# Optimization experiments

Hardware: AMD Instinct MI355X
Metric: run time of the kernel (lower is better)

Reference implementation:

```python
import jax, jax.numpy as jnp
import numpy as np

N_NODES = 50000
N_EDGES = 800000
R = 3          # relations
D_IN = 96
D_HID = 96
D_OUT = 64


def setup_inputs() -> dict:
    key = jax.random.key(0)
    ks = jax.random.split(key, 10)
    s_in = 1.0 / np.sqrt(D_IN)
    s_hid = 1.0 / np.sqrt(D_HID)
    return {
        "x": jax.random.normal(ks[0], (N_NODES, D_IN), jnp.float32),
        "src": jax.random.randint(ks[1], (R, N_EDGES), 0, N_NODES, jnp.int32),
        "dst": jax.random.randint(ks[2], (R, N_EDGES), 0, N_NODES, jnp.int32),
        "Ws1": jax.random.normal(ks[3], (R, D_IN, D_HID), jnp.float32) * s_in,
        "Wn1": jax.random.normal(ks[4], (R, D_IN, D_HID), jnp.float32) * s_in,
        "b1": jnp.zeros((R, D_HID), jnp.float32),
        "Ws2": jax.random.normal(ks[5], (R, D_HID, D_OUT), jnp.float32) * s_hid,
        "Wn2": jax.random.normal(ks[6], (R, D_HID, D_OUT), jnp.float32) * s_hid,
        "b2": jnp.zeros((R, D_OUT), jnp.float32),
    }


def reference(x, src, dst, Ws1, Wn1, b1, Ws2, Wn2, b2):
    N = x.shape[0]
    # in-degree per relation, clamped to 1 (DGL zero-in-degree convention)
    deg = jax.vmap(lambda d: jax.ops.segment_sum(
        jnp.ones(d.shape[0], x.dtype), d, num_segments=N))(dst)        # [R, N]
    inv_deg = (1.0 / jnp.maximum(deg, 1.0))[..., None]                 # [R, N, 1]

    def sage_layer(h, Ws, Wn, b):
        # gather src feats, mean-aggregate onto dst, per relation
        neigh = jax.vmap(lambda s, d: jax.ops.segment_sum(
            h[s], d, num_segments=N))(src, dst) * inv_deg              # [R, N, Din]
        out = jnp.tanh(
            jnp.einsum('nd,rdh->rnh', h, Ws)
            + jnp.einsum('rnd,rdh->rnh', neigh, Wn)
            + b[:, None, :])                                           # [R, N, H]
        return out.mean(axis=0)  # HeteroGraphConv aggregate='mean'

    h1 = sage_layer(x, Ws1, Wn1, b1)
    return sage_layer(h1, Ws2, Wn2, b2)
```

## Files before the change

kernel.cpp:

```cpp
#include <hip/hip_runtime.h>
#include <hip/hip_bf16.h>

constexpr int NN   = 50000;
constexpr int NE   = 800000;
constexpr int NR   = 3;
constexpr int DIN  = 96;
constexpr int DH   = 96;
constexpr int DOUT = 64;
constexpr int SLOT = 64;
constexpr int ZROW = NN;

constexpr int NBUCK   = 196;
constexpr int LCAP    = 56;
constexpr int P1B     = 256;
constexpr int CHUNK   = NE / P1B;
constexpr int BSTRIDE = 3200;
constexpr int LSTRIDE = 200;

constexpr int SCAT_BLKS = NR * P1B;
constexpr int CONV_BLKS = (NN * 96 + 4095) / 4096;
constexpr int WT_ELEMS  = 2 * NR * DIN * DH + 2 * NR * DH * DOUT;
constexpr int WT_BLKS   = (WT_ELEMS + 511) / 512;
constexpr int PREP_GRID = SCAT_BLKS + CONV_BLKS + WT_BLKS;

typedef __attribute__((ext_vector_type(8))) short bf16x8;
typedef __attribute__((ext_vector_type(4))) float f32x4;

__device__ __forceinline__ unsigned short f2b(float f) {
    unsigned int u = __float_as_uint(f);
    u += 0x7fffu + ((u >> 16) & 1u);
    return (unsigned short)(u >> 16);
}
__device__ __forceinline__ float blo(unsigned int u) { return __uint_as_float(u << 16); }
__device__ __forceinline__ float bhi(unsigned int u) { return __uint_as_float(u & 0xffff0000u); }
__device__ __forceinline__ unsigned int pack2(float lo, float hi) {
    return (unsigned int)f2b(lo) | ((unsigned int)f2b(hi) << 16);
}

struct __align__(4) U3 { unsigned int x, y, z; };

__global__ __launch_bounds__(512)
void prep_kernel(const int* __restrict__ src,
                 const int* __restrict__ dst,
                 unsigned int* __restrict__ gbuck,
                 int* __restrict__ glofs,
                 const float* __restrict__ x,
                 unsigned short* __restrict__ xb,
                 const float* __restrict__ Ws1, const float* __restrict__ Wn1,
                 const float* __restrict__ Ws2, const float* __restrict__ Wn2,
                 unsigned short* __restrict__ wt)
{
    __shared__ unsigned int lbuf[NBUCK][LCAP];
    __shared__ int lcnt[NBUCK];
    __shared__ int sa[256], sb[256];
    __shared__ int lofs[NBUCK + 1];

    const int bid = blockIdx.x;
    const int tid = threadIdx.x;

    if (bid < SCAT_BLKS) {
        const int r = bid >> 8, c = bid & 255;
        for (int i = tid; i < NBUCK; i += 512) lcnt[i] = 0;
        __syncthreads();

        const int* sr = src + (size_t)r * NE + (size_t)c * CHUNK;
        const int* dr = dst + (size_t)r * NE + (size_t)c * CHUNK;
        for (int i = tid; i < CHUNK; i += 512) {
            int d = dr[i];
            int s = sr[i];
            int b = d >> 8;
            int pos = atomicAdd(&lcnt[b], 1);
            if (pos < LCAP)
                lbuf[b][pos] = ((unsigned int)(d & 255) << 16) | (unsigned int)s;
        }
        __syncthreads();

        if (tid < 256)
            sa[tid] = (tid < NBUCK) ? min(lcnt[tid], LCAP) : 0;
        __syncthreads();
        int* cur = sa; int* nxt = sb;
        for (int st = 1; st < 256; st <<= 1) {
            if (tid < 256) {
                int v = cur[tid];
                if (tid >= st) v += cur[tid - st];
                nxt[tid] = v;
            }
            __syncthreads();
            int* t2 = cur; cur = nxt; nxt = t2;
        }
        if (tid == 0) lofs[0] = 0;
        if (tid < NBUCK) lofs[tid + 1] = cur[tid];
        __syncthreads();

        if (tid < NBUCK + 1) glofs[(size_t)bid * LSTRIDE + tid] = lofs[tid];

        const int w = tid >> 6, l = tid & 63;
        unsigned int* gb = gbuck + (size_t)bid * BSTRIDE;
        for (int b = w; b < NBUCK; b += 8) {
            int cnt = min(lcnt[b], LCAP);
            if (l < cnt) gb[lofs[b] + l] = lbuf[b][l];
        }
    } else if (bid < SCAT_BLKS + CONV_BLKS) {
        const int rb = bid - SCAT_BLKS;
        if (rb == 0 && tid < 48) {
            unsigned int* z = reinterpret_cast<unsigned int*>(xb + (size_t)ZROW * 96);
            z[tid] = 0u;
        }
        int i = (rb * 512 + tid) * 8;
        if (i < NN * 96) {
            float4 a = *reinterpret_cast<const float4*>(x + i);
            float4 b = *reinterpret_cast<const float4*>(x + i + 4);
            uint4 o;
            o.x = pack2(a.x, a.y);
            o.y = pack2(a.z, a.w);
            o.z = pack2(b.x, b.y);
            o.w = pack2(b.z, b.w);
            *reinterpret_cast<uint4*>(xb + i) = o;
        }
    } else {
        int g = (bid - SCAT_BLKS - CONV_BLKS) * 512 + tid;
        if (g < WT_ELEMS) {
            constexpr int SZ1 = NR * DIN * DH;
            constexpr int SZ2 = NR * DH * DOUT;
            const float* in;
            int idx, KD, ND;
            if (g < SZ1)                { in = Ws1; idx = g;                KD = DIN; ND = DH; }
            else if (g < 2 * SZ1)       { in = Wn1; idx = g - SZ1;          KD = DIN; ND = DH; }
            else if (g < 2 * SZ1 + SZ2) { in = Ws2; idx = g - 2 * SZ1;      KD = DH;  ND = DOUT; }
            else                        { in = Wn2; idx = g - 2 * SZ1 - SZ2; KD = DH; ND = DOUT; }
            int k = idx % KD;
            int rn = idx / KD;
            int n = rn % ND;
            int r = rn / ND;
            wt[g] = f2b(in[((size_t)r * KD + k) * ND + n]);
        }
    }
}

__global__ __launch_bounds__(512)
void bin_build_kernel(const unsigned int* __restrict__ gbuck,
                      const int* __restrict__ glofs,
                      unsigned short* __restrict__ slots,
                      int* __restrict__ deg)
{
    __shared__ unsigned short lslot[256][SLOT];
    __shared__ int lcnt[256];

    const int rb = blockIdx.x;
    const int r  = rb / NBUCK, b = rb - r * NBUCK;
    const int nbase = b * 256;
    int nb = NN - nbase; if (nb > 256) nb = 256;
    const int tid = threadIdx.x;

    unsigned int* ls32i = reinterpret_cast<unsigned int*>(&lslot[0][0]);
    for (int i = tid; i < 256 * SLOT / 2; i += 512) ls32i[i] = 0xC350C350u;
    for (int i = tid; i < 256; i += 512) lcnt[i] = 0;
    __syncthreads();

    const int blk  = tid >> 1;
    const int half = tid & 1;
    const int gblk = r * P1B + blk;
    int o0 = glofs[(size_t)gblk * LSTRIDE + b];
    int o1 = glofs[(size_t)gblk * LSTRIDE + b + 1];
    const unsigned int* run = gbuck + (size_t)gblk * BSTRIDE + o0;
    int cnt = o1 - o0;
    for (int i = half; i < cnt; i += 2) {
        unsigned int e = run[i];
        int nl = e >> 16;
        int pos = atomicAdd(&lcnt[nl], 1);
        if (pos < SLOT) lslot[nl][pos] = (unsigned short)(e & 0xffffu);
    }
    __syncthreads();

    for (int j = tid; j < nb; j += 512) deg[r * NN + nbase + j] = lcnt[j];

    const unsigned int* ls32 = reinterpret_cast<const unsigned int*>(&lslot[0][0]);
    unsigned int* gs32 = reinterpret_cast<unsigned int*>(
        slots + ((size_t)r * NN + nbase) * SLOT);
    const int tot = nb * (SLOT / 2);
    for (int i = tid; i < tot; i += 512) gs32[i] = ls32[i];
}

__global__ __launch_bounds__(256)
void agg_kernel(const unsigned int* __restrict__ Hb,
                const unsigned short* __restrict__ slots,
                const int* __restrict__ deg,
                unsigned int* __restrict__ aggb)
{
    int gid = blockIdx.x * 256 + threadIdx.x;
    int grp = gid >> 4, t = gid & 15;
    if (grp >= NR * NN) return;
    const uint4* sl4 = reinterpret_cast<const uint4*>(slots + (size_t)grp * SLOT);
    int e = deg[grp];
    if (e > SLOT) e = SLOT;

    uint4 iv0 = sl4[0], iv1 = sl4[1], iv2 = sl4[2], iv3 = sl4[3];

    float a0 = 0.f, a1 = 0.f, a2 = 0.f, a3 = 0.f, a4 = 0.f, a5 = 0.f;

#define DO8(V)                                                                 \
    {                                                                          \
        unsigned int i0 = (V).x & 0xffffu, i1 = (V).x >> 16;                   \
        unsigned int i2 = (V).y & 0xffffu, i3 = (V).y >> 16;                   \
        unsigned int i4 = (V).z & 0xffffu, i5 = (V).z >> 16;                   \
        unsigned int i6 = (V).w & 0xffffu, i7 = (V).w >> 16;                   \
        U3 g0 = *reinterpret_cast<const U3*>(Hb + (size_t)i0 * 48 + 3 * t);    \
        U3 g1 = *reinterpret_cast<const U3*>(Hb + (size_t)i1 * 48 + 3 * t);    \
        U3 g2 = *reinterpret_cast<const U3*>(Hb + (size_t)i2 * 48 + 3 * t);    \
        U3 g3 = *reinterpret_cast<const U3*>(Hb + (size_t)i3 * 48 + 3 * t);    \
        U3 g4 = *reinterpret_cast<const U3*>(Hb + (size_t)i4 * 48 + 3 * t);    \
        U3 g5 = *reinterpret_cast<const U3*>(Hb + (size_t)i5 * 48 + 3 * t);    \
        U3 g6 = *reinterpret_cast<const U3*>(Hb + (size_t)i6 * 48 + 3 * t);    \
        U3 g7 = *reinterpret_cast<const U3*>(Hb + (size_t)i7 * 48 + 3 * t);    \
        a0 += blo(g0.x) + blo(g1.x) + blo(g2.x) + blo(g3.x)                    \
            + blo(g4.x) + blo(g5.x) + blo(g6.x) + blo(g7.x);                   \
        a1 += bhi(g0.x) + bhi(g1.x) + bhi(g2.x) + bhi(g3.x)                    \
            + bhi(g4.x) + bhi(g5.x) + bhi(g6.x) + bhi(g7.x);                   \
        a2 += blo(g0.y) + blo(g1.y) + blo(g2.y) + blo(g3.y)                    \
            + blo(g4.y) + blo(g5.y) + blo(g6.y) + blo(g7.y);                   \
        a3 += bhi(g0.y) + bhi(g1.y) + bhi(g2.y) + bhi(g3.y)                    \
            + bhi(g4.y) + bhi(g5.y) + bhi(g6.y) + bhi(g7.y);                   \
        a4 += blo(g0.z) + blo(g1.z) + blo(g2.z) + blo(g3.z)                    \
            + blo(g4.z) + blo(g5.z) + blo(g6.z) + blo(g7.z);                   \
        a5 += bhi(g0.z) + bhi(g1.z) + bhi(g2.z) + bhi(g3.z)                    \
            + bhi(g4.z) + bhi(g5.z) + bhi(g6.z) + bhi(g7.z);                   \
    }

    int nb8 = (e + 7) >> 3;
    if (nb8 > 0) DO8(iv0);
    if (nb8 > 1) DO8(iv1);
    if (nb8 > 2) DO8(iv2);
    if (nb8 > 3) DO8(iv3);
    for (int i = 32; i < e; i += 8) {
        uint4 v = sl4[i >> 3];
        DO8(v);
    }
#undef DO8

    float inv = 1.0f / (float)(e > 0 ? e : 1);
    unsigned int* o = aggb + (size_t)grp * 48 + 3 * t;
    o[0] = pack2(a0 * inv, a1 * inv);
    o[1] = pack2(a2 * inv, a3 * inv);
    o[2] = pack2(a4 * inv, a5 * inv);
}

template <int NOUT, bool OUT16>
__global__ __launch_bounds__(256)
void mfma_layer_kernel(const unsigned short* Hb,
                       const unsigned short* __restrict__ aggb,
                       const unsigned short* __restrict__ Wts,
                       const unsigned short* __restrict__ Wtn,
                       const float* __restrict__ bias,
                       unsigned short* o16,
                       float* __restrict__ o32)
{
    const int w    = threadIdx.x >> 6;
    const int l    = threadIdx.x & 63;
    const int n0   = blockIdx.x * 64 + w * 16;
    const int arow = l & 15, asel = l >> 4;
    int na = n0 + arow;
    if (na > NN - 1) na = NN - 1;

    bf16x8 ax[3], ag[NR][3];
    {
        const unsigned short* xr = Hb + (size_t)na * 96 + asel * 8;
        #pragma unroll
        for (int kb = 0; kb < 3; ++kb)
            ax[kb] = *reinterpret_cast<const bf16x8*>(xr + kb * 32);
        #pragma unroll
        for (int r = 0; r < NR; ++r) {
            const unsigned short* gr = aggb + ((size_t)r * NN + na) * 96 + asel * 8;
            #pragma unroll
            for (int kb = 0; kb < 3; ++kb)
                ag[r][kb] = *reinterpret_cast<const bf16x8*>(gr + kb * 32);
        }
    }

    constexpr int NC = NOUT / 16;
    #pragma unroll
    for (int c = 0; c < NC; ++c) {
        f32x4 acc[NR];
        #pragma unroll
        for (int r = 0; r < NR; ++r) acc[r] = (f32x4){0.f, 0.f, 0.f, 0.f};

        #pragma unroll
        for (int r = 0; r < NR; ++r) {
            const unsigned short* bs = Wts + ((size_t)r * NOUT + c * 16 + arow) * 96 + asel * 8;
            const unsigned short* bn = Wtn + ((size_t)r * NOUT + c * 16 + arow) * 96 + asel * 8;
            #pragma unroll
            for (int kb = 0; kb < 3; ++kb) {
                acc[r] = __builtin_amdgcn_mfma_f32_16x16x32_bf16(
                    ax[kb], *reinterpret_cast<const bf16x8*>(bs + kb * 32), acc[r], 0, 0, 0);
                acc[r] = __builtin_amdgcn_mfma_f32_16x16x32_bf16(
                    ag[r][kb], *reinterpret_cast<const bf16x8*>(bn + kb * 32), acc[r], 0, 0, 0);
            }
        }

        const int col = c * 16 + arow;
        const float b0 = bias[col];
        const float b1 = bias[NOUT + col];
        const float b2 = bias[2 * NOUT + col];
        #pragma unroll
        for (int j = 0; j < 4; ++j) {
            int node = n0 + asel * 4 + j;
            if (node < NN) {
                float v = (tanhf(acc[0][j] + b0) + tanhf(acc[1][j] + b1)
                         + tanhf(acc[2][j] + b2)) * (1.0f / 3.0f);
                if (OUT16) o16[(size_t)node * 96 + col] = f2b(v);
                else       o32[(size_t)node * DOUT + col] = v;
            }
        }
    }
}

extern "C" void kernel_launch(void* const* d_in, const int* in_sizes, int n_in,
                              void* d_out, int out_size, void* d_ws, size_t ws_size,
                              hipStream_t stream)
{
    const float* x   = (const float*)d_in[0];
    const int*   src = (const int*)d_in[1];
    const int*   dst = (const int*)d_in[2];
    const float* Ws1 = (const float*)d_in[3];
    const float* Wn1 = (const float*)d_in[4];
    const float* b1  = (const float*)d_in[5];
    const float* Ws2 = (const float*)d_in[6];
    const float* Wn2 = (const float*)d_in[7];
    const float* b2  = (const float*)d_in[8];
    float* out = (float*)d_out;

    char* ws = (char*)d_ws;
    size_t o = 0;
    auto alloc = [&](size_t bytes) {
        size_t p = o;
        o += (bytes + 255) & ~(size_t)255;
        return p;
    };
    int* deg = (int*)(ws + alloc((size_t)NR * NN * 4));
    unsigned short* slots = (unsigned short*)(ws + alloc((size_t)NR * NN * SLOT * 2));
    unsigned short* xb = (unsigned short*)(ws + alloc((size_t)(NN + 1) * 96 * 2));
    unsigned short* aggb = (unsigned short*)(ws + alloc((size_t)NR * NN * 96 * 2));
    unsigned short* wt = (unsigned short*)(ws + alloc((size_t)WT_ELEMS * 2));
    unsigned short* wt1s = wt;
    unsigned short* wt1n = wt1s + NR * DIN * DH;
    unsigned short* wt2s = wt1n + NR * DIN * DH;
    unsigned short* wt2n = wt2s + NR * DH * DOUT;
    unsigned int* gbuck = (unsigned int*)aggb;
    int* glofs = (int*)((char*)aggb + (size_t)NR * P1B * BSTRIDE * 4);

    prep_kernel<<<PREP_GRID, 512, 0, stream>>>(
        src, dst, gbuck, glofs, x, xb, Ws1, Wn1, Ws2, Wn2, wt);

    bin_build_kernel<<<NR * NBUCK, 512, 0, stream>>>(gbuck, glofs, slots, deg);

    constexpr int AGG_GRID  = NR * NN * 16 / 256;
    constexpr int GEMM_GRID = (NN + 63) / 64;

    agg_kernel<<<AGG_GRID, 256, 0, stream>>>(
        (const unsigned int*)xb, slots, deg, (unsigned int*)aggb);
    mfma_layer_kernel<DH, true><<<GEMM_GRID, 256, 0, stream>>>(
        xb, aggb, wt1s, wt1n, b1, xb, (float*)nullptr);

    agg_kernel<<<AGG_GRID, 256, 0, stream>>>(
        (const unsigned int*)xb, slots, deg, (unsigned int*)aggb);
    mfma_layer_kernel<DOUT, false><<<GEMM_GRID, 256, 0, stream>>>(
        xb, aggb, wt2s, wt2n, b2, (unsigned short*)nullptr, out);
}
```

Measured before the change: 210.8 us.

## Transform-before-aggregate in layer 2 and degree-sorted aggregation ordering

Layer 2 now projects h1 through Wn2 per relation first (y2_kernel, 96 to 64 features) and then gathers and averages the 64-wide rows, exploiting linearity of mean aggregation. This shrinks gather traffic and removes the neighbor MFMAs from the final layer kernel, at the cost of an extra GEMM pass and an intermediate buffer. It also adds per-bucket sorting of nodes by in-degree in bin_build, and the aggregation kernels walk nodes in that order so wavefronts see similar degrees and diverge less. The fast path runs only if the workspace is large enough, with a fallback to the old path otherwise.

```diff
diff --git a/kernel.cpp b/kernel.cpp
--- a/kernel.cpp
+++ b/kernel.cpp
@@ -16,6 +16,7 @@
 constexpr int CHUNK   = NE / P1B;
 constexpr int BSTRIDE = 3200;
 constexpr int LSTRIDE = 200;
+constexpr int NWIN    = NR * NBUCK;
 
 constexpr int SCAT_BLKS = NR * P1B;
 constexpr int CONV_BLKS = (NN * 96 + 4095) / 4096;
@@ -124,10 +125,10 @@
             constexpr int SZ2 = NR * DH * DOUT;
             const float* in;
             int idx, KD, ND;
-            if (g < SZ1)                { in = Ws1; idx = g;                KD = DIN; ND = DH; }
-            else if (g < 2 * SZ1)       { in = Wn1; idx = g - SZ1;          KD = DIN; ND = DH; }
-            else if (g < 2 * SZ1 + SZ2) { in = Ws2; idx = g - 2 * SZ1;      KD = DH;  ND = DOUT; }
-            else                        { in = Wn2; idx = g - 2 * SZ1 - SZ2; KD = DH; ND = DOUT; }
+            if (g < SZ1)                { in = Ws1; idx = g;                 KD = DIN; ND = DH; }
+            else if (g < 2 * SZ1)       { in = Wn1; idx = g - SZ1;           KD = DIN; ND = DH; }
+            else if (g < 2 * SZ1 + SZ2) { in = Ws2; idx = g - 2 * SZ1;       KD = DH;  ND = DOUT; }
+            else                        { in = Wn2; idx = g - 2 * SZ1 - SZ2; KD = DH;  ND = DOUT; }
             int k = idx % KD;
             int rn = idx / KD;
             int n = rn % ND;
@@ -141,10 +142,12 @@
 void bin_build_kernel(const unsigned int* __restrict__ gbuck,
                       const int* __restrict__ glofs,
                       unsigned short* __restrict__ slots,
-                      int* __restrict__ deg)
+                      int* __restrict__ deg,
+                      unsigned short* __restrict__ order)
 {
     __shared__ unsigned short lslot[256][SLOT];
     __shared__ int lcnt[256];
+    __shared__ unsigned short sord[256];
 
     const int rb = blockIdx.x;
     const int r  = rb / NBUCK, b = rb - r * NBUCK;
@@ -155,6 +158,7 @@
     unsigned int* ls32i = reinterpret_cast<unsigned int*>(&lslot[0][0]);
     for (int i = tid; i < 256 * SLOT / 2; i += 512) ls32i[i] = 0xC350C350u;
     for (int i = tid; i < 256; i += 512) lcnt[i] = 0;
+    if (tid < 128) reinterpret_cast<unsigned int*>(sord)[tid] = 0xFFFFFFFFu;
     __syncthreads();
 
     const int blk  = tid >> 1;
@@ -174,6 +178,23 @@
 
     for (int j = tid; j < nb; j += 512) deg[r * NN + nbase + j] = lcnt[j];
 
+    if (tid < 256) {
+        const int j = tid;
+        const int myk = (j < nb) ? lcnt[j] : -1;
+        int rank = 0;
+        #pragma unroll 8
+        for (int k = 0; k < 256; ++k) {
+            int kk = (k < nb) ? lcnt[k] : -1;
+            rank += (kk > myk) || (kk == myk && k < j);
+        }
+        if (j < nb) sord[rank] = (unsigned short)j;
+    }
+    __syncthreads();
+
+    if (tid < 128)
+        reinterpret_cast<unsigned int*>(order + (size_t)rb * 256)[tid] =
+            reinterpret_cast<const unsigned int*>(sord)[tid];
+
     const unsigned int* ls32 = reinterpret_cast<const unsigned int*>(&lslot[0][0]);
     unsigned int* gs32 = reinterpret_cast<unsigned int*>(
         slots + ((size_t)r * NN + nbase) * SLOT);
@@ -181,21 +202,35 @@
     for (int i = tid; i < tot; i += 512) gs32[i] = ls32[i];
 }
 
+__device__ __forceinline__ bool agg_decode(const unsigned short* __restrict__ order,
+                                           int g, int& r, int& node, int& grp)
+{
+    int rb = g >> 8;
+    int ordv = order[g];
+    if (ordv == 0xFFFF) return false;
+    r = rb / NBUCK;
+    int b = rb - r * NBUCK;
+    node = (b << 8) + ordv;
+    grp = r * NN + node;
+    return true;
+}
+
 __global__ __launch_bounds__(256)
-void agg_kernel(const unsigned int* __restrict__ Hb,
-                const unsigned short* __restrict__ slots,
-                const int* __restrict__ deg,
-                unsigned int* __restrict__ aggb)
+void agg96_kernel(const unsigned int* __restrict__ Hb,
+                  const unsigned short* __restrict__ slots,
+                  const int* __restrict__ deg,
+                  const unsigned short* __restrict__ order,
+                  unsigned int* __restrict__ aggb)
 {
     int gid = blockIdx.x * 256 + threadIdx.x;
-    int grp = gid >> 4, t = gid & 15;
-    if (grp >= NR * NN) return;
+    int g = gid >> 4, t = gid & 15;
+    int r, node, grp;
+    if (!agg_decode(order, g, r, node, grp)) return;
     const uint4* sl4 = reinterpret_cast<const uint4*>(slots + (size_t)grp * SLOT);
     int e = deg[grp];
     if (e > SLOT) e = SLOT;
 
     uint4 iv0 = sl4[0], iv1 = sl4[1], iv2 = sl4[2], iv3 = sl4[3];
-
     float a0 = 0.f, a1 = 0.f, a2 = 0.f, a3 = 0.f, a4 = 0.f, a5 = 0.f;
 
 #define DO8(V)                                                                 \
@@ -244,16 +279,76 @@
     o[2] = pack2(a4 * inv, a5 * inv);
 }
 
-template <int NOUT, bool OUT16>
 __global__ __launch_bounds__(256)
-void mfma_layer_kernel(const unsigned short* Hb,
-                       const unsigned short* __restrict__ aggb,
-                       const unsigned short* __restrict__ Wts,
-                       const unsigned short* __restrict__ Wtn,
-                       const float* __restrict__ bias,
-                       unsigned short* o16,
-                       float* __restrict__ o32)
-{
+void agg64_kernel(const unsigned int* __restrict__ y2,
+                  const unsigned short* __restrict__ slots,
+                  const int* __restrict__ deg,
+                  const unsigned short* __restrict__ order,
+                  unsigned int* __restrict__ aggY2)
+{
+    int gid = blockIdx.x * 256 + threadIdx.x;
+    int g = gid >> 4, t = gid & 15;
+    int r, node, grp;
+    if (!agg_decode(order, g, r, node, grp)) return;
+    const unsigned int* Tp = y2 + (size_t)r * ((size_t)(NN + 1) * 32);
+    const uint4* sl4 = reinterpret_cast<const uint4*>(slots + (size_t)grp * SLOT);
+    int e = deg[grp];
+    if (e > SLOT) e = SLOT;
+
+    uint4 iv0 = sl4[0], iv1 = sl4[1], iv2 = sl4[2], iv3 = sl4[3];
+    float a0 = 0.f, a1 = 0.f, a2 = 0.f, a3 = 0.f;
+
+#define DO8W(V)                                                                \
+    {                                                                          \
+        unsigned int i0 = (V).x & 0xffffu, i1 = (V).x >> 16;                   \
+        unsigned int i2 = (V).y & 0xffffu, i3 = (V).y >> 16;                   \
+        unsigned int i4 = (V).z & 0xffffu, i5 = (V).z >> 16;                   \
+        unsigned int i6 = (V).w & 0xffffu, i7 = (V).w >> 16;                   \
+        uint2 g0 = *reinterpret_cast<const uint2*>(Tp + (size_t)i0 * 32 + 2 * t); \
+        uint2 g1 = *reinterpret_cast<const uint2*>(Tp + (size_t)i1 * 32 + 2 * t); \
+        uint2 g2 = *reinterpret_cast<const uint2*>(Tp + (size_t)i2 * 32 + 2 * t); \
+        uint2 g3 = *reinterpret_cast<const uint2*>(Tp + (size_t)i3 * 32 + 2 * t); \
+        uint2 g4 = *reinterpret_cast<const uint2*>(Tp + (size_t)i4 * 32 + 2 * t); \
+        uint2 g5 = *reinterpret_cast<const uint2*>(Tp + (size_t)i5 * 32 + 2 * t); \
+        uint2 g6 = *reinterpret_cast<const uint2*>(Tp + (size_t)i6 * 32 + 2 * t); \
+        uint2 g7 = *reinterpret_cast<const uint2*>(Tp + (size_t)i7 * 32 + 2 * t); \
+        a0 += blo(g0.x) + blo(g1.x) + blo(g2.x) + blo(g3.x)                    \
+            + blo(g4.x) + blo(g5.x) + blo(g6.x) + blo(g7.x);                   \
+        a1 += bhi(g0.x) + bhi(g1.x) + bhi(g2.x) + bhi(g3.x)                    \
+            + bhi(g4.x) + bhi(g5.x) + bhi(g6.x) + bhi(g7.x);                   \
+        a2 += blo(g0.y) + blo(g1.y) + blo(g2.y) + blo(g3.y)                    \
+            + blo(g4.y) + blo(g5.y) + blo(g6.y) + blo(g7.y);                   \
+        a3 += bhi(g0.y) + bhi(g1.y) + bhi(g2.y) + bhi(g3.y)                    \
+            + bhi(g4.y) + bhi(g5.y) + bhi(g6.y) + bhi(g7.y);                   \
+    }
+
+    int nb8 = (e + 7) >> 3;
+    if (nb8 > 0) DO8W(iv0);
+    if (nb8 > 1) DO8W(iv1);
+    if (nb8 > 2) DO8W(iv2);
+    if (nb8 > 3) DO8W(iv3);
+    for (int i = 32; i < e; i += 8) {
+        uint4 v = sl4[i >> 3];
+        DO8W(v);
+    }
+#undef DO8W
+
+    float inv = 1.0f / (float)(e > 0 ? e : 1);
+    unsigned int* o = aggY2 + (size_t)grp * 32 + 2 * t;
+    o[0] = pack2(a0 * inv, a1 * inv);
+    o[1] = pack2(a2 * inv, a3 * inv);
+}
+
+__global__ __launch_bounds__(256)
+void y2_kernel(const unsigned short* __restrict__ Hb,
+               const unsigned short* __restrict__ Wtn,
+               unsigned short* __restrict__ y2)
+{
+    if (blockIdx.x == 0 && threadIdx.x < 96) {
+        unsigned int* z = reinterpret_cast<unsigned int*>(y2);
+        int r = threadIdx.x >> 5, d = threadIdx.x & 31;
+        z[((size_t)r * (NN + 1) + ZROW) * 32 + d] = 0u;
+    }
     const int w    = threadIdx.x >> 6;
     const int l    = threadIdx.x & 63;
     const int n0   = blockIdx.x * 64 + w * 16;
@@ -261,42 +356,107 @@
     int na = n0 + arow;
     if (na > NN - 1) na = NN - 1;
 
+    bf16x8 ax[3];
+    const unsigned short* xr = Hb + (size_t)na * 96 + asel * 8;
+    #pragma unroll
+    for (int kb = 0; kb < 3; ++kb)
+        ax[kb] = *reinterpret_cast<const bf16x8*>(xr + kb * 32);
+
+    #pragma unroll
+    for (int c = 0; c < 4; ++c) {
+        f32x4 acc[NR];
+        #pragma unroll
+        for (int r = 0; r < NR; ++r) acc[r] = (f32x4){0.f, 0.f, 0.f, 0.f};
+        #pragma unroll
+        for (int r = 0; r < NR; ++r) {
+            const unsigned short* bn = Wtn + ((size_t)r * DOUT + c * 16 + arow) * 96 + asel * 8;
+            #pragma unroll
+            for (int kb = 0; kb < 3; ++kb)
+                acc[r] = __builtin_amdgcn_mfma_f32_16x16x32_bf16(
+                    ax[kb], *reinterpret_cast<const bf16x8*>(bn + kb * 32), acc[r], 0, 0, 0);
+        }
+        const int col = c * 16 + arow;
+        #pragma unroll
+        for (int r = 0; r < NR; ++r)
+            #pragma unroll
+            for (int j = 0; j < 4; ++j) {
+                int node = n0 + asel * 4 + j;
+                if (node < NN)
+                    y2[((size_t)r * (NN + 1) + node) * 64 + col] = f2b(acc[r][j]);
+            }
+    }
+}
+
+template <int NOUT, bool OUT16, bool PRE_AGG>
+__global__ __launch_bounds__(256)
+void mfma_layer_kernel(const unsigned short* Hb,
+                       const unsigned short* __restrict__ aggb,
+                       const unsigned short* __restrict__ aggY2,
+                       const unsigned short* __restrict__ Wts,
+                       const unsigned short* __restrict__ Wtn,
+                       const float* __restrict__ bias,
+                       unsigned short* o16,
+                       float* __restrict__ o32)
+{
+    const int w    = threadIdx.x >> 6;
+    const int l    = threadIdx.x & 63;
+    const int n0   = blockIdx.x * 64 + w * 16;
+    const int arow = l & 15, asel = l >> 4;
+    int na = n0 + arow;
+    if (na > NN - 1) na = NN - 1;
+
     bf16x8 ax[3], ag[NR][3];
     {
         const unsigned short* xr = Hb + (size_t)na * 96 + asel * 8;
         #pragma unroll
         for (int kb = 0; kb < 3; ++kb)
             ax[kb] = *reinterpret_cast<const bf16x8*>(xr + kb * 32);
-        #pragma unroll
-        for (int r = 0; r < NR; ++r) {
-            const unsigned short* gr = aggb + ((size_t)r * NN + na) * 96 + asel * 8;
+        if (!PRE_AGG) {
             #pragma unroll
-            for (int kb = 0; kb < 3; ++kb)
-                ag[r][kb] = *reinterpret_cast<const bf16x8*>(gr + kb * 32);
+            for (int r = 0; r < NR; ++r) {
+                const unsigned short* gr = aggb + ((size_t)r * NN + na) * 96 + asel * 8;
+                #pragma unroll
+                for (int kb = 0; kb < 3; ++kb)
+                    ag[r][kb] = *reinterpret_cast<const bf16x8*>(gr + kb * 32);
+            }
         }
     }
 
     constexpr int NC = NOUT / 16;
     #pragma unroll
     for (int c = 0; c < NC; ++c) {
+        const int col = c * 16 + arow;
         f32x4 acc[NR];
-        #pragma unroll
-        for (int r = 0; r < NR; ++r) acc[r] = (f32x4){0.f, 0.f, 0.f, 0.f};
+        if (PRE_AGG) {
+            #pragma unroll
+            for (int r = 0; r < NR; ++r)
+                #pragma unroll
+                for (int j = 0; j < 4; ++j) {
+                    int nj = n0 + asel * 4 + j;
+                    if (nj > NN - 1) nj = NN - 1;
+                    unsigned short hv = aggY2[((size_t)r * NN + nj) * NOUT + col];
+                    acc[r][j] = __uint_as_float((unsigned int)hv << 16);
+                }
+        } else {
+            #pragma unroll
+            for (int r = 0; r < NR; ++r) acc[r] = (f32x4){0.f, 0.f, 0.f, 0.f};
+        }
 
         #pragma unroll
         for (int r = 0; r < NR; ++r) {
             const unsigned short* bs = Wts + ((size_t)r * NOUT + c * 16 + arow) * 96 + asel * 8;
-            const unsigned short* bn = Wtn + ((size_t)r * NOUT + c * 16 + arow) * 96 + asel * 8;
             #pragma unroll
             for (int kb = 0; kb < 3; ++kb) {
                 acc[r] = __builtin_amdgcn_mfma_f32_16x16x32_bf16(
                     ax[kb], *reinterpret_cast<const bf16x8*>(bs + kb * 32), acc[r], 0, 0, 0);
-                acc[r] = __builtin_amdgcn_mfma_f32_16x16x32_bf16(
-                    ag[r][kb], *reinterpret_cast<const bf16x8*>(bn + kb * 32), acc[r], 0, 0, 0);
+                if (!PRE_AGG) {
+                    const unsigned short* bn = Wtn + ((size_t)r * NOUT + c * 16 + arow) * 96 + asel * 8;
+                    acc[r] = __builtin_amdgcn_mfma_f32_16x16x32_bf16(
+                        ag[r][kb], *reinterpret_cast<const bf16x8*>(bn + kb * 32), acc[r], 0, 0, 0);
+                }
             }
         }
 
-        const int col = c * 16 + arow;
         const float b0 = bias[col];
         const float b1 = bias[NOUT + col];
         const float b2 = bias[2 * NOUT + col];
@@ -340,28 +500,43 @@
     unsigned short* xb = (unsigned short*)(ws + alloc((size_t)(NN + 1) * 96 * 2));
     unsigned short* aggb = (unsigned short*)(ws + alloc((size_t)NR * NN * 96 * 2));
     unsigned short* wt = (unsigned short*)(ws + alloc((size_t)WT_ELEMS * 2));
+    unsigned short* order = (unsigned short*)(ws + alloc((size_t)NWIN * 256 * 2));
+    size_t need_base = o;
+    unsigned short* aggY2 = (unsigned short*)(ws + alloc((size_t)NR * NN * DOUT * 2));
+    size_t need_fast = o;
+    const bool fast2 = (ws_size >= need_fast);
+    (void)need_base;
+
     unsigned short* wt1s = wt;
     unsigned short* wt1n = wt1s + NR * DIN * DH;
     unsigned short* wt2s = wt1n + NR * DIN * DH;
     unsigned short* wt2n = wt2s + NR * DH * DOUT;
     unsigned int* gbuck = (unsigned int*)aggb;
     int* glofs = (int*)((char*)aggb + (size_t)NR * P1B * BSTRIDE * 4);
+    unsigned short* y2 = aggb;
 
     prep_kernel<<<PREP_GRID, 512, 0, stream>>>(
         src, dst, gbuck, glofs, x, xb, Ws1, Wn1, Ws2, Wn2, wt);
-
-    bin_build_kernel<<<NR * NBUCK, 512, 0, stream>>>(gbuck, glofs, slots, deg);
-
-    constexpr int AGG_GRID  = NR * NN * 16 / 256;
+    bin_build_kernel<<<NWIN, 512, 0, stream>>>(gbuck, glofs, slots, deg, order);
+
+    constexpr int AGG_GRID  = NWIN * 16;
     constexpr int GEMM_GRID = (NN + 63) / 64;
 
-    agg_kernel<<<AGG_GRID, 256, 0, stream>>>(
-        (const unsigned int*)xb, slots, deg, (unsigned int*)aggb);
-    mfma_layer_kernel<DH, true><<<GEMM_GRID, 256, 0, stream>>>(
-        xb, aggb, wt1s, wt1n, b1, xb, (float*)nullptr);
-
-    agg_kernel<<<AGG_GRID, 256, 0, stream>>>(
-        (const unsigned int*)xb, slots, deg, (unsigned int*)aggb);
-    mfma_layer_kernel<DOUT, false><<<GEMM_GRID, 256, 0, stream>>>(
-        xb, aggb, wt2s, wt2n, b2, (unsigned short*)nullptr, out);
-}
+    agg96_kernel<<<AGG_GRID, 256, 0, stream>>>(
+        (const unsigned int*)xb, slots, deg, order, (unsigned int*)aggb);
+    mfma_layer_kernel<DH, true, false><<<GEMM_GRID, 256, 0, stream>>>(
+        xb, aggb, nullptr, wt1s, wt1n, b1, xb, (float*)nullptr);
+
+    if (fast2) {
+        y2_kernel<<<GEMM_GRID, 256, 0, stream>>>(xb, wt2n, y2);
+        agg64_kernel<<<AGG_GRID, 256, 0, stream>>>(
+            (const unsigned int*)y2, slots, deg, order, (unsigned int*)aggY2);
+        mfma_layer_kernel<DOUT, false, true><<<GEMM_GRID, 256, 0, stream>>>(
+            xb, nullptr, aggY2, wt2s, wt2n, b2, (unsigned short*)nullptr, out);
+    } else {
+        agg96_kernel<<<AGG_GRID, 256, 0, stream>>>(
+            (const unsigned int*)xb, slots, deg, order, (unsigned int*)aggb);
+        mfma_layer_kernel<DOUT, false, false><<<GEMM_GRID, 256, 0, stream>>>(
+            xb, aggb, nullptr, wt2s, wt2n, b2, (unsigned short*)nullptr, out);
+    }
+}
```

Result: slower. 225.7 us (+7.0%).

## Slice aggregation by feature column across XCD-mapped blocks for L2 locality

Applied to the files above, without the earlier changes.

Replaces the aggregation kernel with a column-sliced version. Each block handles one third of the 96-wide feature row (16 dwords) for 16 destination groups. The block index is mapped so that blocks landing on different XCDs (blockIdx mod 8) work on a fixed slice, so each XCD's L2 caches only part of the source feature table. Slot-index loads and output stores become nontemporal to avoid polluting cache. The cost is three times as many slot/degree reads and a smaller 4-byte gather per lane, which may lower memory-level parallelism per thread.

```diff
diff --git a/kernel.cpp b/kernel.cpp
--- a/kernel.cpp
+++ b/kernel.cpp
@@ -23,8 +23,13 @@
 constexpr int WT_BLKS   = (WT_ELEMS + 511) / 512;
 constexpr int PREP_GRID = SCAT_BLKS + CONV_BLKS + WT_BLKS;
 
+constexpr int NGRP_BLKS  = NR * NN / 16;
+constexpr int AGG_ROUNDS = (NGRP_BLKS + 1) / 2;
+constexpr int AGGS_GRID  = AGG_ROUNDS * 8;
+
 typedef __attribute__((ext_vector_type(8))) short bf16x8;
 typedef __attribute__((ext_vector_type(4))) float f32x4;
+typedef __attribute__((ext_vector_type(4))) unsigned int uint4v;
 
 __device__ __forceinline__ unsigned short f2b(float f) {
     unsigned int u = __float_as_uint(f);
@@ -36,8 +41,6 @@
 __device__ __forceinline__ unsigned int pack2(float lo, float hi) {
     return (unsigned int)f2b(lo) | ((unsigned int)f2b(hi) << 16);
 }
-
-struct __align__(4) U3 { unsigned int x, y, z; };
 
 __global__ __launch_bounds__(512)
 void prep_kernel(const int* __restrict__ src,
@@ -124,10 +127,10 @@
             constexpr int SZ2 = NR * DH * DOUT;
             const float* in;
             int idx, KD, ND;
-            if (g < SZ1)                { in = Ws1; idx = g;                KD = DIN; ND = DH; }
-            else if (g < 2 * SZ1)       { in = Wn1; idx = g - SZ1;          KD = DIN; ND = DH; }
-            else if (g < 2 * SZ1 + SZ2) { in = Ws2; idx = g - 2 * SZ1;      KD = DH;  ND = DOUT; }
-            else                        { in = Wn2; idx = g - 2 * SZ1 - SZ2; KD = DH; ND = DOUT; }
+            if (g < SZ1)                { in = Ws1; idx = g;                 KD = DIN; ND = DH; }
+            else if (g < 2 * SZ1)       { in = Wn1; idx = g - SZ1;           KD = DIN; ND = DH; }
+            else if (g < 2 * SZ1 + SZ2) { in = Ws2; idx = g - 2 * SZ1;       KD = DH;  ND = DOUT; }
+            else                        { in = Wn2; idx = g - 2 * SZ1 - SZ2; KD = DH;  ND = DOUT; }
             int k = idx % KD;
             int rn = idx / KD;
             int n = rn % ND;
@@ -182,66 +185,69 @@
 }
 
 __global__ __launch_bounds__(256)
-void agg_kernel(const unsigned int* __restrict__ Hb,
-                const unsigned short* __restrict__ slots,
-                const int* __restrict__ deg,
-                unsigned int* __restrict__ aggb)
-{
-    int gid = blockIdx.x * 256 + threadIdx.x;
-    int grp = gid >> 4, t = gid & 15;
-    if (grp >= NR * NN) return;
-    const uint4* sl4 = reinterpret_cast<const uint4*>(slots + (size_t)grp * SLOT);
+void agg_sliced_kernel(const unsigned int* __restrict__ Hb,
+                       const unsigned short* __restrict__ slots,
+                       const int* __restrict__ deg,
+                       unsigned int* __restrict__ aggb)
+{
+    const int x = blockIdx.x & 7;
+    const int q = blockIdx.x >> 3;
+    const int s = (x * 3) >> 3;
+    const int nx = (s == 2) ? 2 : 3;
+    const int k = x - ((s == 0) ? 0 : (s == 1) ? 3 : 6);
+    const int j = q * nx + k;
+    if (j >= NGRP_BLKS) return;
+
+    const int tid = threadIdx.x;
+    const int grp = j * 16 + (tid >> 4);
+    const int t   = tid & 15;
+    const unsigned int* T = Hb + s * 16 + t;
+
+    const uint4v* sl4 = reinterpret_cast<const uint4v*>(slots + (size_t)grp * SLOT);
     int e = deg[grp];
     if (e > SLOT) e = SLOT;
 
-    uint4 iv0 = sl4[0], iv1 = sl4[1], iv2 = sl4[2], iv3 = sl4[3];
-
-    float a0 = 0.f, a1 = 0.f, a2 = 0.f, a3 = 0.f, a4 = 0.f, a5 = 0.f;
-
-#define DO8(V)                                                                 \
+    uint4v iv0 = __builtin_nontemporal_load(sl4 + 0);
+    uint4v iv1 = __builtin_nontemporal_load(sl4 + 1);
+    uint4v iv2 = __builtin_nontemporal_load(sl4 + 2);
+    uint4v iv3 = __builtin_nontemporal_load(sl4 + 3);
+
+    float a0 = 0.f, a1 = 0.f;
+
+#define DO8S(V)                                                                \
     {                                                                          \
         unsigned int i0 = (V).x & 0xffffu, i1 = (V).x >> 16;                   \
         unsigned int i2 = (V).y & 0xffffu, i3 = (V).y >> 16;                   \
         unsigned int i4 = (V).z & 0xffffu, i5 = (V).z >> 16;                   \
         unsigned int i6 = (V).w & 0xffffu, i7 = (V).w >> 16;                   \
-        U3 g0 = *reinterpret_cast<const U3*>(Hb + (size_t)i0 * 48 + 3 * t);    \
-        U3 g1 = *reinterpret_cast<const U3*>(Hb + (size_t)i1 * 48 + 3 * t);    \
-        U3 g2 = *reinterpret_cast<const U3*>(Hb + (size_t)i2 * 48 + 3 * t);    \
-        U3 g3 = *reinterpret_cast<const U3*>(Hb + (size_t)i3 * 48 + 3 * t);    \
-        U3 g4 = *reinterpret_cast<const U3*>(Hb + (size_t)i4 * 48 + 3 * t);    \
-        U3 g5 = *reinterpret_cast<const U3*>(Hb + (size_t)i5 * 48 + 3 * t);    \
-        U3 g6 = *reinterpret_cast<const U3*>(Hb + (size_t)i6 * 48 + 3 * t);    \
-        U3 g7 = *reinterpret_cast<const U3*>(Hb + (size_t)i7 * 48 + 3 * t);    \
-        a0 += blo(g0.x) + blo(g1.x) + blo(g2.x) + blo(g3.x)                    \
-            + blo(g4.x) + blo(g5.x) + blo(g6.x) + blo(g7.x);                   \
-        a1 += bhi(g0.x) + bhi(g1.x) + bhi(g2.x) + bhi(g3.x)                    \
-            + bhi(g4.x) + bhi(g5.x) + bhi(g6.x) + bhi(g7.x);                   \
-        a2 += blo(g0.y) + blo(g1.y) + blo(g2.y) + blo(g3.y)                    \
-            + blo(g4.y) + blo(g5.y) + blo(g6.y) + blo(g7.y);                   \
-        a3 += bhi(g0.y) + bhi(g1.y) + bhi(g2.y) + bhi(g3.y)                    \
-            + bhi(g4.y) + bhi(g5.y) + bhi(g6.y) + bhi(g7.y);                   \
-        a4 += blo(g0.z) + blo(g1.z) + blo(g2.z) + blo(g3.z)                    \
-            + blo(g4.z) + blo(g5.z) + blo(g6.z) + blo(g7.z);                   \
-        a5 += bhi(g0.z) + bhi(g1.z) + bhi(g2.z) + bhi(g3.z)                    \
-            + bhi(g4.z) + bhi(g5.z) + bhi(g6.z) + bhi(g7.z);                   \
+        unsigned int u0 = T[(size_t)i0 * 48];                                  \
+        unsigned int u1 = T[(size_t)i1 * 48];                                  \
+        unsigned int u2 = T[(size_t)i2 * 48];                                  \
+        unsigned int u3 = T[(size_t)i3 * 48];                                  \
+        unsigned int u4 = T[(size_t)i4 * 48];                                  \
+        unsigned int u5 = T[(size_t)i5 * 48];                                  \
+        unsigned int u6 = T[(size_t)i6 * 48];                                  \
+        unsigned int u7 = T[(size_t)i7 * 48];                                  \
+        a0 += blo(u0) + blo(u1) + blo(u2) + blo(u3)                            \
+            + blo(u4) + blo(u5) + blo(u6) + blo(u7);                           \
+        a1 += bhi(u0) + bhi(u1) + bhi(u2) + bhi(u3)                            \
+            + bhi(u4) + bhi(u5) + bhi(u6) + bhi(u7);                           \
     }
 
     int nb8 = (e + 7) >> 3;
-    if (nb8 > 0) DO8(iv0);
-    if (nb8 > 1) DO8(iv1);
-    if (nb8 > 2) DO8(iv2);
-    if (nb8 > 3) DO8(iv3);
+    if (nb8 > 0) DO8S(iv0);
+    if (nb8 > 1) DO8S(iv1);
+    if (nb8 > 2) DO8S(iv2);
+    if (nb8 > 3) DO8S(iv3);
     for (int i = 32; i < e; i += 8) {
-        uint4 v = sl4[i >> 3];
-        DO8(v);
-    }
-#undef DO8
+        uint4v v = __builtin_nontemporal_load(sl4 + (i >> 3));
+        DO8S(v);
+    }
+#undef DO8S
 
     float inv = 1.0f / (float)(e > 0 ? e : 1);
-    unsigned int* o = aggb + (size_t)grp * 48 + 3 * t;
-    o[0] = pack2(a0 * inv, a1 * inv);
-    o[1] = pack2(a2 * inv, a3 * inv);
-    o[2] = pack2(a4 * inv, a5 * inv);
+    __builtin_nontemporal_store(pack2(a0 * inv, a1 * inv),
+                                &aggb[(size_t)grp * 48 + s * 16 + t]);
 }
 
 template <int NOUT, bool OUT16>
@@ -338,29 +344,29 @@
     int* deg = (int*)(ws + alloc((size_t)NR * NN * 4));
     unsigned short* slots = (unsigned short*)(ws + alloc((size_t)NR * NN * SLOT * 2));
     unsigned short* xb = (unsigned short*)(ws + alloc((size_t)(NN + 1) * 96 * 2));
-    unsigned short* aggb = (unsigned short*)(ws + alloc((size_t)NR * NN * 96 * 2));
+    char* aggregion = ws + alloc((size_t)NR * NN * 96 * 2);
     unsigned short* wt = (unsigned short*)(ws + alloc((size_t)WT_ELEMS * 2));
     unsigned short* wt1s = wt;
     unsigned short* wt1n = wt1s + NR * DIN * DH;
     unsigned short* wt2s = wt1n + NR * DIN * DH;
     unsigned short* wt2n = wt2s + NR * DH * DOUT;
-    unsigned int* gbuck = (unsigned int*)aggb;
-    int* glofs = (int*)((char*)aggb + (size_t)NR * P1B * BSTRIDE * 4);
+
+    unsigned int* gbuck = (unsigned int*)aggregion;
+    int* glofs = (int*)(aggregion + (size_t)NR * P1B * BSTRIDE * 4);
+    unsigned short* aggb = (unsigned short*)aggregion;
 
     prep_kernel<<<PREP_GRID, 512, 0, stream>>>(
         src, dst, gbuck, glofs, x, xb, Ws1, Wn1, Ws2, Wn2, wt);
-
     bin_build_kernel<<<NR * NBUCK, 512, 0, stream>>>(gbuck, glofs, slots, deg);
 
-    constexpr int AGG_GRID  = NR * NN * 16 / 256;
     constexpr int GEMM_GRID = (NN + 63) / 64;
 
-    agg_kernel<<<AGG_GRID, 256, 0, stream>>>(
+    agg_sliced_kernel<<<AGGS_GRID, 256, 0, stream>>>(
         (const unsigned int*)xb, slots, deg, (unsigned int*)aggb);
     mfma_layer_kernel<DH, true><<<GEMM_GRID, 256, 0, stream>>>(
         xb, aggb, wt1s, wt1n, b1, xb, (float*)nullptr);
 
-    agg_kernel<<<AGG_GRID, 256, 0, stream>>>(
+    agg_sliced_kernel<<<AGGS_GRID, 256, 0, stream>>>(
         (const unsigned int*)xb, slots, deg, (unsigned int*)aggb);
     mfma_layer_kernel<DOUT, false><<<GEMM_GRID, 256, 0, stream>>>(
         xb, aggb, wt2s, wt2n, b2, (unsigned short*)nullptr, out);
```

Measured after the change: 304.5 us. +44.5%, slower.
